# Kernel tuning notes

Hardware: AMD Instinct MI355X
Metric: run time of the kernel (lower is better)

Reference implementation:

```python
import jax, jax.numpy as jnp
import numpy as np

T, C_IN, H, W = 128, 3, 64, 64
HC = (32, 64)
K = 3


def _conv(x, w, b):
    # x: [1, Cin, H, W], w: [Cout, Cin, K, K] -> SAME padding
    y = jax.lax.conv_general_dilated(
        x, w, window_strides=(1, 1), padding='SAME',
        dimension_numbers=('NCHW', 'OIHW', 'NCHW'))
    return y + b[None, :, None, None]


def _run_layer(xs, w, b, hc):
    # xs: [T, Cin, H, W]; scan the ConvLSTM cell over time (batch = 1)
    h0 = jnp.zeros((1, hc, xs.shape[-2], xs.shape[-1]), xs.dtype)
    c0 = jnp.zeros_like(h0)

    def step(carry, x):
        h, c = carry
        z = _conv(jnp.concatenate([x[None], h], axis=1), w, b)  # [1, 4*hc, H, W]
        i, f, o, g = jnp.split(z, 4, axis=1)
        c_next = jax.nn.sigmoid(f) * c + jax.nn.sigmoid(i) * jnp.tanh(g)
        h_next = jax.nn.sigmoid(o) * jnp.tanh(c_next)
        return (h_next, c_next), h_next[0]

    (h, c), ys = jax.lax.scan(step, (h0, c0), xs)
    return ys, h, c  # ys: [T, hc, H, W]


def setup_inputs() -> dict:
    key = jax.random.key(0)
    ks = jax.random.split(key, 4)
    inp = {
        'input': jax.random.normal(ks[0], (T, C_IN, H, W), jnp.float32),
        'w1': jax.random.normal(ks[1], (4 * HC[0], C_IN + HC[0], K, K), jnp.float32) * 0.05,
        'b1': jnp.zeros((4 * HC[0],), jnp.float32),
        'w2': jax.random.normal(ks[2], (4 * HC[1], HC[0] + HC[1], K, K), jnp.float32) * 0.05,
        'b2': jnp.zeros((4 * HC[1],), jnp.float32),
        'fc_w': jax.random.uniform(ks[3], (6, H * W * HC[1]), jnp.float32, -0.1, 0.1),
        'fc_b': jnp.zeros((6,), jnp.float32),
    }
    return inp


def reference(input, w1, b1, w2, b2, fc_w, fc_b):
    ys1, h1, c1 = _run_layer(input, w1, b1, HC[0])
    ys2, h2, c2 = _run_layer(ys1, w2, b2, HC[1])
    outputs = ys2.reshape(ys2.shape[0], -1)          # [T, hc2*H*W]
    pose_sequence = outputs @ fc_w.T + fc_b          # [T, 6]
    return pose_sequence, h1, c1, h2, c2
```

## Files before the change

kernel.cpp:

```cpp
#include <hip/hip_runtime.h>

typedef _Float16 f16;
typedef _Float16 f16x8 __attribute__((ext_vector_type(8)));
typedef float f32x4 __attribute__((ext_vector_type(4)));
typedef unsigned short ushort_t;
typedef unsigned long long u64_t;


#define IN1SZ 209088
#define IN2BSZ 278784
#define WP1OFF 975744
#define WP1SZ 73728
#define WP2OFF (WP1OFF + WP1SZ)
#define WP2SZ 221184
#define FCWPOFF (WP2OFF + WP2SZ)

__device__ __forceinline__ float sigm(float x) {
  return __builtin_amdgcn_rcpf(1.0f + __expf(-x));
}
__device__ __forceinline__ float tanh_fast(float x) {
  float xc = fminf(fmaxf(x, -10.f), 10.f);
  float e = __expf(2.f * xc);
  return (e - 1.f) * __builtin_amdgcn_rcpf(e + 1.f);
}
__device__ __forceinline__ ushort_t f2u(f16 v) { return __builtin_bit_cast(ushort_t, v); }
__device__ __forceinline__ f16x8 u2f(uint4 v) { return __builtin_bit_cast(f16x8, v); }

__global__ __launch_bounds__(256) void pack_kernel(const float* __restrict__ w1,
                                                   const float* __restrict__ w2,
                                                   const float* __restrict__ fcb,
                                                   const float* __restrict__ x0,
                                                   const float* __restrict__ fcw,
                                                   float* __restrict__ pose,
                                                   ushort_t* __restrict__ wp1,
                                                   ushort_t* __restrict__ wp2,
                                                   ushort_t* __restrict__ in1hi0,
                                                   float* __restrict__ fcwp) {
  int i = blockIdx.x * 256 + threadIdx.x;
  if (i < 27648) {
    int lane = i & 63;
    int f = i >> 6;
    int mt = f & 7;
    int sm = f >> 3;
    int s = sm % 27, mb = sm / 27;
    int m = mt * 16 + (lane & 15);
    int rg = mb * 128 + m;
    int h = rg >> 2, G = rg & 3;
    int orow = G * 64 + h;
    int tap = s / 3, cb = (s % 3) * 32;
    int cq = cb + (lane >> 4) * 8;
    for (int j = 0; j < 8; ++j) {
      float v = w2[(orow * 96 + cq + j) * 9 + tap];
      wp2[f * 512 + lane * 8 + j] = f2u((f16)v);
    }
    return;
  }
  i -= 27648;
  if (i < 9216) {
    int lane = i & 63;
    int f = i >> 6;
    int mt = f & 3;
    int sm = f >> 2;
    int s = sm % 18, mb = sm / 18;
    int m = mt * 16 + (lane & 15);
    int rg = mb * 64 + m;
    int h = rg >> 2, G = rg & 3;
    int orow = G * 32 + h;
    int tap = s >> 1, cb = (s & 1) * 32;
    int cq = cb + (lane >> 4) * 8;
    for (int j = 0; j < 8; ++j) {
      int c = cq + j;
      float v = 0.f;
      if (c < 32) v = w1[(orow * 35 + c + 3) * 9 + tap];
      else if (c < 35) v = w1[(orow * 35 + c - 32) * 9 + tap];
      wp1[f * 512 + lane * 8 + j] = f2u((f16)v);
    }
    return;
  }
  i -= 9216;
  if (i < 768) { pose[i] = fcb[i % 6]; return; }
  i -= 768;
  if (i < 12288) {
    int c = i >> 12, pix = i & 4095;
    int y = pix >> 6, x = pix & 63;
    int pidx = ((y + 1) * 66 + (x + 1)) * 48 + 32 + c;
    in1hi0[pidx] = f2u((f16)x0[i]);
    return;
  }
  i -= 12288;
  if (i < 262144) {
    float* dst = fcwp + (size_t)i * 6;
#pragma unroll
    for (int j = 0; j < 6; ++j) dst[j] = fcw[(size_t)j * 262144 + i];
  }
}

template <int LAYER>
__device__ __forceinline__ void conv_body(
    int bid,
    const ushort_t* __restrict__ bhi, const ushort_t* __restrict__ b2hi,
    const ushort_t* __restrict__ wp, const float* __restrict__ bias,
    float* __restrict__ cst, float* __restrict__ hout,
    ushort_t* __restrict__ d1hi,
    const float* __restrict__ fcwp, float* __restrict__ pose_t,
    const float* __restrict__ xn,
    ushort_t* Bh, ushort_t* hs, float (*red)[6]) {
  constexpr int CS = (LAYER == 1) ? 72 : 104;
  constexpr int NC32 = (LAYER == 1) ? 2 : 3;
  constexpr int NS = 9 * NC32;
  constexpr int MT = (LAYER == 1) ? 4 : 8;
  constexpr int MTPW = (LAYER == 1) ? 1 : 2;
  constexpr int H = (LAYER == 1) ? 32 : 64;
  constexpr int DEPTH = 8;
  constexpr int PRE = DEPTH - 1;

  const int tid = threadIdx.x;
  const int lane = tid & 63;
  const int w = tid >> 6;
  const int mb = bid & 1;
  const int ntile = bid >> 1;
  const int Y0 = (ntile >> 3) * 4;
  const int X0 = (ntile & 7) * 8;

  if (LAYER == 2) {
    for (int i = tid; i < 720; i += 256) {
      int hy = i / 120, rem = i % 120;
      int hx = rem / 12, c8 = rem % 12;
      int pos = (Y0 + hy) * 66 + X0 + hx;
      int dst = (hy * 10 + hx) * CS + c8 * 8;
      if (c8 < 4) {
        *(uint4*)(&Bh[dst]) = *(const uint4*)(&bhi[pos * 48 + c8 * 8]);
      } else {
        *(uint4*)(&Bh[dst]) = *(const uint4*)(&b2hi[pos * 64 + (c8 - 4) * 8]);
      }
    }
  } else {
    for (int i = tid; i < 360; i += 256) {
      int hy = i / 60, rem = i % 60;
      int hx = rem / 6, c8 = (rem % 6) * 8;
      int src = ((Y0 + hy) * 66 + X0 + hx) * 48 + c8;
      int dst = (hy * 10 + hx) * CS + c8;
      *(uint4*)(&Bh[dst]) = *(const uint4*)(&bhi[src]);
    }
    for (int i = tid; i < 120; i += 256) {
      int hp = i >> 1;
      int dst = hp * CS + 48 + (i & 1) * 8;
      *(uint4*)(&Bh[dst]) = uint4{0, 0, 0, 0};
    }
  }

  const ushort_t* aptr[MTPW];
#pragma unroll
  for (int m = 0; m < MTPW; ++m) {
    int f = (mb * NS) * MT + (w * MTPW + m);
    aptr[m] = wp + f * 512 + lane * 8;
  }
  uint4 A[DEPTH][MTPW];
  auto loada = [&](int s) {
#pragma unroll
    for (int m = 0; m < MTPW; ++m) {
      A[s % DEPTH][m] = *(const uint4*)(aptr[m] + (size_t)s * (MT * 512));
    }
  };
#pragma unroll
  for (int s = 0; s < PRE; ++s) loada(s);
  __syncthreads();

  const int n = lane & 15;
  const int q = lane >> 4;
  const int py = n >> 3, px = n & 7;

  f32x4 acc[MTPW][2];
#pragma unroll
  for (int m = 0; m < MTPW; ++m)
#pragma unroll
    for (int nt = 0; nt < 2; ++nt) acc[m][nt] = f32x4{0.f, 0.f, 0.f, 0.f};

#pragma unroll
  for (int s = 0; s < NS; ++s) {
    if (s + PRE < NS) loada(s + PRE);
    const int tap = s / NC32, cc = s % NC32;
    const int ty = tap / 3, tx = tap % 3;
    const int coff = cc * 32 + q * 8;
    f16x8 bfh[2];
#pragma unroll
    for (int nt = 0; nt < 2; ++nt) {
      int hp = (py + nt * 2 + ty) * 10 + (px + tx);
      bfh[nt] = u2f(*(const uint4*)(&Bh[hp * CS + coff]));
    }
#pragma unroll
    for (int m = 0; m < MTPW; ++m) {
      f16x8 ah = u2f(A[s % DEPTH][m]);
#pragma unroll
      for (int nt = 0; nt < 2; ++nt) {
        acc[m][nt] = __builtin_amdgcn_mfma_f32_16x16x32_f16(ah, bfh[nt], acc[m][nt], 0, 0, 0);
      }
    }
  }

  float p6[6] = {0, 0, 0, 0, 0, 0};
#pragma unroll
  for (int m = 0; m < MTPW; ++m) {
    const int ch = (w * MTPW + m) * 4 + q;
    const int hg = mb * (MT * 4) + ch;
    const float bi = bias[0 * H + hg];
    const float bf = bias[1 * H + hg];
    const float bo = bias[2 * H + hg];
    const float bg = bias[3 * H + hg];
#pragma unroll
    for (int nt = 0; nt < 2; ++nt) {
      const int pI = nt * 16 + n;
      float zi = acc[m][nt][0] + bi;
      float zf = acc[m][nt][1] + bf;
      float zo = acc[m][nt][2] + bo;
      float zg = acc[m][nt][3] + bg;
      int y = Y0 + (pI >> 3), x = X0 + (pI & 7);
      int cidx = hg * 4096 + y * 64 + x;
      float cold = cst[cidx];
      float cn = sigm(zf) * cold + sigm(zi) * tanh_fast(zg);
      float hn = sigm(zo) * tanh_fast(cn);
      cst[cidx] = cn;
      hout[cidx] = hn;
      hs[pI * 36 + ch] = f2u((f16)hn);
      if (LAYER == 2) {
#pragma unroll
        for (int j = 0; j < 6; ++j) p6[j] += hn * fcwp[(size_t)cidx * 6 + j];
      }
    }
  }
  __syncthreads();

  if (LAYER == 2) {
    int pxi = tid & 31, g = tid >> 5;
    int y = Y0 + (pxi >> 3), x = X0 + (pxi & 7);
    int pidx = (y + 1) * 66 + (x + 1);
    u64_t v = *(const u64_t*)&hs[pxi * 36 + g * 4];
    *(u64_t*)&d1hi[pidx * 64 + mb * 32 + g * 4] = v;
  } else {
    if (tid < 128) {
      int pxi = tid & 31, g = tid >> 5;
      int y = Y0 + (pxi >> 3), x = X0 + (pxi & 7);
      int pidx = (y + 1) * 66 + (x + 1);
      u64_t v = *(const u64_t*)&hs[pxi * 36 + g * 4];
      *(u64_t*)&d1hi[pidx * 48 + mb * 16 + g * 4] = v;
    }
    if (mb == 0 && tid >= 128 && tid < 160) {
      int t2 = tid - 128;
      int yy = Y0 + (t2 >> 3), xx = X0 + (t2 & 7);
      int pidx2 = (yy + 1) * 66 + (xx + 1);
#pragma unroll
      for (int c = 0; c < 3; ++c) {
        d1hi[pidx2 * 48 + 32 + c] = f2u((f16)xn[c * 4096 + yy * 64 + xx]);
      }
    }
  }

  if (LAYER == 2) {
#pragma unroll
    for (int j = 0; j < 6; ++j)
#pragma unroll
      for (int off = 32; off > 0; off >>= 1) p6[j] += __shfl_xor(p6[j], off, 64);
    if (lane == 0)
#pragma unroll
      for (int j = 0; j < 6; ++j) red[w][j] = p6[j];
    __syncthreads();
    if (tid < 6) atomicAdd(pose_t + tid, red[0][tid] + red[1][tid] + red[2][tid] + red[3][tid]);
  }
}

__global__ __launch_bounds__(256, 2) void fused_step(
    int t,
    const ushort_t* __restrict__ i1rhi, ushort_t* __restrict__ i1whi,
    const ushort_t* __restrict__ i2brhi, ushort_t* __restrict__ i2bwhi,
    const ushort_t* __restrict__ wp1, const ushort_t* __restrict__ wp2,
    const float* __restrict__ b1, const float* __restrict__ b2,
    float* __restrict__ c1o, float* __restrict__ h1o,
    float* __restrict__ c2o, float* __restrict__ h2o,
    const float* __restrict__ fcwp, float* __restrict__ pose_t,
    const float* __restrict__ xn) {
  __shared__ __align__(16) ushort_t Bh[6240];
  __shared__ __align__(8) ushort_t hs[1152];
  __shared__ float red[4][6];

  int bid = blockIdx.x;
  if (bid < 256) {
    if (t >= 128) return;
    conv_body<1>(bid, i1rhi, nullptr, wp1, b1, c1o, h1o,
                 i1whi,
                 nullptr, nullptr, xn, Bh, hs, red);
  } else {
    if (t < 1) return;
    conv_body<2>(bid - 256, i1rhi, i2brhi, wp2, b2, c2o, h2o,
                 i2bwhi,
                 fcwp, pose_t, nullptr, Bh, hs, red);
  }
}

extern "C" void kernel_launch(void* const* d_in, const int* in_sizes, int n_in, void* d_out,
                              int out_size, void* d_ws, size_t ws_size, hipStream_t stream) {
  const float* input = (const float*)d_in[0];
  const float* w1 = (const float*)d_in[1];
  const float* b1 = (const float*)d_in[2];
  const float* w2 = (const float*)d_in[3];
  const float* b2 = (const float*)d_in[4];
  const float* fcw = (const float*)d_in[5];
  const float* fcb = (const float*)d_in[6];

  float* out = (float*)d_out;
  float* pose = out;
  float* h1o = out + 768;
  float* c1o = h1o + 131072;
  float* h2o = c1o + 131072;
  float* c2o = h2o + 262144;

  ushort_t* ws = (ushort_t*)d_ws;
  ushort_t* in1hi[2] = {ws, ws + IN1SZ};
  ushort_t* bb = ws + 2 * IN1SZ;
  ushort_t* i2bhi[2] = {bb, bb + IN2BSZ};
  ushort_t* wp1 = ws + WP1OFF;
  ushort_t* wp2 = ws + WP2OFF;
  float* fcwp = (float*)(ws + FCWPOFF);

  hipMemsetAsync(ws, 0, (size_t)WP1OFF * 2, stream);
  hipMemsetAsync(c1o, 0, (size_t)655360 * 4, stream);
  pack_kernel<<<1219, 256, 0, stream>>>(w1, w2, fcb, input, fcw, pose, wp1, wp2,
                                        in1hi[0], fcwp);

  for (int t = 0; t <= 128; ++t) {
    int p = t & 1, pn = p ^ 1;
    int tn = (t + 1 < 128) ? t + 1 : 127;
    float* pose_t = pose + ((t > 0) ? (t - 1) * 6 : 0);
    fused_step<<<512, 256, 0, stream>>>(
        t,
        in1hi[p], in1hi[pn],
        i2bhi[pn], i2bhi[p],
        wp1, wp2, b1, b2, c1o, h1o, c2o, h2o,
        fcwp, pose_t,
        input + (size_t)tn * 12288);
  }
}
```

Before: 1.531 ms.

## Retile layer-2 conv to 16 gate rows by 64 pixels per block

```diff
diff --git a/kernel.cpp b/kernel.cpp
--- a/kernel.cpp
+++ b/kernel.cpp
@@ -40,11 +40,11 @@
   if (i < 27648) {
     int lane = i & 63;
     int f = i >> 6;
-    int mt = f & 7;
-    int sm = f >> 3;
+    int mt = f & 3;
+    int sm = f >> 2;
     int s = sm % 27, mb = sm / 27;
     int m = mt * 16 + (lane & 15);
-    int rg = mb * 128 + m;
+    int rg = mb * 64 + m;
     int h = rg >> 2, G = rg & 3;
     int orow = G * 64 + h;
     int tap = s / 3, cb = (s % 3) * 32;
@@ -108,22 +108,24 @@
   constexpr int CS = (LAYER == 1) ? 72 : 104;
   constexpr int NC32 = (LAYER == 1) ? 2 : 3;
   constexpr int NS = 9 * NC32;
-  constexpr int MT = (LAYER == 1) ? 4 : 8;
-  constexpr int MTPW = (LAYER == 1) ? 1 : 2;
+  constexpr int MT = 4;
   constexpr int H = (LAYER == 1) ? 32 : 64;
+  constexpr int NT = (LAYER == 1) ? 2 : 4;
+  constexpr int TY = (LAYER == 1) ? 4 : 8;
+  constexpr int MBB = (LAYER == 1) ? 1 : 2;
   constexpr int DEPTH = 8;
   constexpr int PRE = DEPTH - 1;
 
   const int tid = threadIdx.x;
   const int lane = tid & 63;
   const int w = tid >> 6;
-  const int mb = bid & 1;
-  const int ntile = bid >> 1;
-  const int Y0 = (ntile >> 3) * 4;
+  const int mb = bid & ((1 << MBB) - 1);
+  const int ntile = bid >> MBB;
+  const int Y0 = (ntile >> 3) * TY;
   const int X0 = (ntile & 7) * 8;
 
   if (LAYER == 2) {
-    for (int i = tid; i < 720; i += 256) {
+    for (int i = tid; i < (TY + 2) * 10 * 12; i += 256) {
       int hy = i / 120, rem = i % 120;
       int hx = rem / 12, c8 = rem % 12;
       int pos = (Y0 + hy) * 66 + X0 + hx;
@@ -149,18 +151,10 @@
     }
   }
 
-  const ushort_t* aptr[MTPW];
-#pragma unroll
-  for (int m = 0; m < MTPW; ++m) {
-    int f = (mb * NS) * MT + (w * MTPW + m);
-    aptr[m] = wp + f * 512 + lane * 8;
-  }
-  uint4 A[DEPTH][MTPW];
+  const ushort_t* aptr = wp + ((mb * NS) * MT + w) * 512 + lane * 8;
+  uint4 A[DEPTH];
   auto loada = [&](int s) {
-#pragma unroll
-    for (int m = 0; m < MTPW; ++m) {
-      A[s % DEPTH][m] = *(const uint4*)(aptr[m] + (size_t)s * (MT * 512));
-    }
+    A[s % DEPTH] = *(const uint4*)(aptr + (size_t)s * (MT * 512));
   };
 #pragma unroll
   for (int s = 0; s < PRE; ++s) loada(s);
@@ -170,11 +164,9 @@
   const int q = lane >> 4;
   const int py = n >> 3, px = n & 7;
 
-  f32x4 acc[MTPW][2];
-#pragma unroll
-  for (int m = 0; m < MTPW; ++m)
-#pragma unroll
-    for (int nt = 0; nt < 2; ++nt) acc[m][nt] = f32x4{0.f, 0.f, 0.f, 0.f};
+  f32x4 acc[NT];
+#pragma unroll
+  for (int nt = 0; nt < NT; ++nt) acc[nt] = f32x4{0.f, 0.f, 0.f, 0.f};
 
 #pragma unroll
   for (int s = 0; s < NS; ++s) {
@@ -182,66 +174,56 @@
     const int tap = s / NC32, cc = s % NC32;
     const int ty = tap / 3, tx = tap % 3;
     const int coff = cc * 32 + q * 8;
-    f16x8 bfh[2];
-#pragma unroll
-    for (int nt = 0; nt < 2; ++nt) {
+    f16x8 ah = u2f(A[s % DEPTH]);
+#pragma unroll
+    for (int nt = 0; nt < NT; ++nt) {
       int hp = (py + nt * 2 + ty) * 10 + (px + tx);
-      bfh[nt] = u2f(*(const uint4*)(&Bh[hp * CS + coff]));
-    }
-#pragma unroll
-    for (int m = 0; m < MTPW; ++m) {
-      f16x8 ah = u2f(A[s % DEPTH][m]);
-#pragma unroll
-      for (int nt = 0; nt < 2; ++nt) {
-        acc[m][nt] = __builtin_amdgcn_mfma_f32_16x16x32_f16(ah, bfh[nt], acc[m][nt], 0, 0, 0);
-      }
+      f16x8 bfh = u2f(*(const uint4*)(&Bh[hp * CS + coff]));
+      acc[nt] = __builtin_amdgcn_mfma_f32_16x16x32_f16(ah, bfh, acc[nt], 0, 0, 0);
     }
   }
 
   float p6[6] = {0, 0, 0, 0, 0, 0};
-#pragma unroll
-  for (int m = 0; m < MTPW; ++m) {
-    const int ch = (w * MTPW + m) * 4 + q;
-    const int hg = mb * (MT * 4) + ch;
-    const float bi = bias[0 * H + hg];
-    const float bf = bias[1 * H + hg];
-    const float bo = bias[2 * H + hg];
-    const float bg = bias[3 * H + hg];
-#pragma unroll
-    for (int nt = 0; nt < 2; ++nt) {
-      const int pI = nt * 16 + n;
-      float zi = acc[m][nt][0] + bi;
-      float zf = acc[m][nt][1] + bf;
-      float zo = acc[m][nt][2] + bo;
-      float zg = acc[m][nt][3] + bg;
-      int y = Y0 + (pI >> 3), x = X0 + (pI & 7);
-      int cidx = hg * 4096 + y * 64 + x;
-      float cold = cst[cidx];
-      float cn = sigm(zf) * cold + sigm(zi) * tanh_fast(zg);
-      float hn = sigm(zo) * tanh_fast(cn);
-      cst[cidx] = cn;
-      hout[cidx] = hn;
-      hs[pI * 36 + ch] = f2u((f16)hn);
-      if (LAYER == 2) {
-#pragma unroll
-        for (int j = 0; j < 6; ++j) p6[j] += hn * fcwp[(size_t)cidx * 6 + j];
-      }
+  const int ch = w * 4 + q;
+  const int hg = mb * 16 + ch;
+  const float bi = bias[0 * H + hg];
+  const float bf = bias[1 * H + hg];
+  const float bo = bias[2 * H + hg];
+  const float bg = bias[3 * H + hg];
+#pragma unroll
+  for (int nt = 0; nt < NT; ++nt) {
+    const int pI = nt * 16 + n;
+    float zi = acc[nt][0] + bi;
+    float zf = acc[nt][1] + bf;
+    float zo = acc[nt][2] + bo;
+    float zg = acc[nt][3] + bg;
+    int y = Y0 + (pI >> 3), x = X0 + (pI & 7);
+    int cidx = hg * 4096 + y * 64 + x;
+    float cold = cst[cidx];
+    float cn = sigm(zf) * cold + sigm(zi) * tanh_fast(zg);
+    float hn = sigm(zo) * tanh_fast(cn);
+    cst[cidx] = cn;
+    hout[cidx] = hn;
+    hs[pI * 20 + ch] = f2u((f16)hn);
+    if (LAYER == 2) {
+#pragma unroll
+      for (int j = 0; j < 6; ++j) p6[j] += hn * fcwp[(size_t)cidx * 6 + j];
     }
   }
   __syncthreads();
 
   if (LAYER == 2) {
-    int pxi = tid & 31, g = tid >> 5;
+    int pxi = tid & 63, g = tid >> 6;
     int y = Y0 + (pxi >> 3), x = X0 + (pxi & 7);
     int pidx = (y + 1) * 66 + (x + 1);
-    u64_t v = *(const u64_t*)&hs[pxi * 36 + g * 4];
-    *(u64_t*)&d1hi[pidx * 64 + mb * 32 + g * 4] = v;
+    u64_t v = *(const u64_t*)&hs[pxi * 20 + g * 4];
+    *(u64_t*)&d1hi[pidx * 64 + mb * 16 + g * 4] = v;
   } else {
     if (tid < 128) {
       int pxi = tid & 31, g = tid >> 5;
       int y = Y0 + (pxi >> 3), x = X0 + (pxi & 7);
       int pidx = (y + 1) * 66 + (x + 1);
-      u64_t v = *(const u64_t*)&hs[pxi * 36 + g * 4];
+      u64_t v = *(const u64_t*)&hs[pxi * 20 + g * 4];
       *(u64_t*)&d1hi[pidx * 48 + mb * 16 + g * 4] = v;
     }
     if (mb == 0 && tid >= 128 && tid < 160) {
@@ -278,8 +260,8 @@
     float* __restrict__ c2o, float* __restrict__ h2o,
     const float* __restrict__ fcwp, float* __restrict__ pose_t,
     const float* __restrict__ xn) {
-  __shared__ __align__(16) ushort_t Bh[6240];
-  __shared__ __align__(8) ushort_t hs[1152];
+  __shared__ __align__(16) ushort_t Bh[10400];
+  __shared__ __align__(8) ushort_t hs[1280];
   __shared__ float red[4][6];
 
   int bid = blockIdx.x;
```

Measured after the change: 1.620 ms. +5.8%, slower.
